# Kernel tuning notes

Hardware: AMD Instinct MI355X
Metric: run time of the kernel (lower is better)

Reference implementation:

```python
import jax, jax.numpy as jnp
import numpy as np

D = 128      # embedding_dim
H = 8        # n_heads
L = 2        # n_encode_layers
FF = 512     # feed-forward hidden (4*D, AM default)
CLIP = 10.0  # tanh_clipping
EPS = 1e-5


def setup_inputs() -> dict:
    key = jax.random.key(0)
    ks = jax.random.split(key, 24)
    B, N = 32, 1000
    Nt = N + 2  # 2 depots + customers

    def w(k, shape, fan_in):
        return (jax.random.normal(k, shape, jnp.float32) / np.float32(np.sqrt(fan_in)))

    inp = {}
    inp["depot"] = jax.random.uniform(ks[0], (B, 2, 2), jnp.float32)
    inp["loc"] = jax.random.uniform(ks[1], (B, N, 2), jnp.float32)
    inp["demand"] = jax.random.uniform(ks[2], (B, N), jnp.float32)
    inp["mask"] = jax.random.randint(ks[3], (B, Nt), 0, 2) == 1
    # init embeddings
    inp["W_init_node"] = w(ks[4], (3, D), 3)
    inp["b_init_node"] = jnp.zeros((D,), jnp.float32)
    inp["W_init_depot"] = w(ks[5], (2, D), 2)
    inp["b_init_depot"] = jnp.zeros((D,), jnp.float32)
    # encoder layers (stacked over L)
    inp["enc_Wqkv"] = w(ks[6], (L, D, 3 * D), D)
    inp["enc_Wo"] = w(ks[7], (L, D, D), D)
    inp["enc_W1"] = w(ks[8], (L, D, FF), D)
    inp["enc_b1"] = jnp.zeros((L, FF), jnp.float32)
    inp["enc_W2"] = w(ks[9], (L, FF, D), FF)
    inp["enc_b2"] = jnp.zeros((L, D), jnp.float32)
    inp["bn1_s"] = jnp.ones((L, D), jnp.float32)
    inp["bn1_b"] = jnp.zeros((L, D), jnp.float32)
    inp["bn2_s"] = jnp.ones((L, D), jnp.float32)
    inp["bn2_b"] = jnp.zeros((L, D), jnp.float32)
    # decoder precompute / pointer attention
    inp["W_proj_node"] = w(ks[10], (D, 3 * D), D)   # project_node_embeddings_p2v
    inp["W_fixed_ctx"] = w(ks[11], (D, D), D)       # project_node_query_context
    inp["W_step_ctx"] = w(ks[12], (D, D), D)        # project_step_context_p2v
    inp["W_out"] = w(ks[13], (D, D), D)             # project_out_p2v
    return inp


def _bn(x, s, b):
    # BatchNorm1d over flattened (batch*nodes), training-mode stats, affine
    m = x.mean((0, 1))
    v = x.var((0, 1))
    return s * (x - m) * jax.lax.rsqrt(v + EPS) + b


def _mha(x, Wqkv, Wo):
    B, N, _ = x.shape
    dk = D // H
    q, k, v = jnp.split(x @ Wqkv, 3, axis=-1)

    def heads(t):
        return t.reshape(B, N, H, dk).transpose(0, 2, 1, 3)  # [B,H,N,dk]

    q, k, v = heads(q), heads(k), heads(v)
    attn = jax.nn.softmax(jnp.einsum('bhqd,bhkd->bhqk', q, k) / np.float32(np.sqrt(dk)), axis=-1)
    o = jnp.einsum('bhqk,bhkd->bhqd', attn, v).transpose(0, 2, 1, 3).reshape(B, N, D)
    return o @ Wo


def reference(depot, loc, demand, mask,
              W_init_node, b_init_node, W_init_depot, b_init_depot,
              enc_Wqkv, enc_Wo, enc_W1, enc_b1, enc_W2, enc_b2,
              bn1_s, bn1_b, bn2_s, bn2_b,
              W_proj_node, W_fixed_ctx, W_step_ctx, W_out):
    B = loc.shape[0]
    NEG = jnp.float32(-1e9)
    # --- init embeddings: depots via Linear(2,D), nodes via Linear(3,D) on (x,y,demand)
    depot_emb = depot @ W_init_depot + b_init_depot                      # [B,2,D]
    node_feat = jnp.concatenate([loc, demand[..., None]], -1)            # [B,N,3]
    node_emb = node_feat @ W_init_node + b_init_node                     # [B,N,D]
    h = jnp.concatenate([depot_emb, node_emb], 1)                        # [B,Nt,D]
    # --- graph encoder: L x (MHA + BN skip, FF + BN skip)
    for l in range(L):
        h = _bn(h + _mha(h, enc_Wqkv[l], enc_Wo[l]), bn1_s[l], bn1_b[l])
        ff = jax.nn.relu(h @ enc_W1[l] + enc_b1[l]) @ enc_W2[l] + enc_b2[l]
        h = _bn(h + ff, bn2_s[l], bn2_b[l])
    # --- fixed precompute (AttentionModelFixed)
    graph_embed = h.mean(1)                                              # [B,D]
    fixed_ctx = graph_embed @ W_fixed_ctx                                # [B,D]
    K_g, V_g, K_logit = jnp.split(h @ W_proj_node, 3, axis=-1)           # each [B,Nt,D]
    dk = D // H
    Kh = K_g.reshape(B, -1, H, dk).transpose(0, 2, 1, 3)                 # [B,H,Nt,dk]
    Vh = V_g.reshape(B, -1, H, dk).transpose(0, 2, 1, 3)
    # --- one glimpse+pointer step: context = fixed + projected first-depot step context
    query = fixed_ctx + h[:, 0, :] @ W_step_ctx                          # [B,D]
    qh = query.reshape(B, H, dk)                                         # [B,H,dk]
    compat = jnp.einsum('bhd,bhnd->bhn', qh, Kh) / np.float32(np.sqrt(dk))
    compat = jnp.where(mask[:, None, :], NEG, compat)                    # mask_inner
    attn = jax.nn.softmax(compat, axis=-1)
    glimpse = jnp.einsum('bhn,bhnd->bhd', attn, Vh).reshape(B, D) @ W_out
    logits = jnp.einsum('bd,bnd->bn', glimpse, K_logit) / np.float32(np.sqrt(D))
    logits = CLIP * jnp.tanh(logits)                                     # tanh clipping
    logits = jnp.where(mask, NEG, logits)                                # mask_logits
    log_p = jax.nn.log_softmax(logits, axis=-1)                          # [B,Nt]
    return log_p
```

## Files before the change

kernel.cpp:

```cpp
#include <hip/hip_runtime.h>

#define B_   32
#define NT_  1002
#define D_   128
#define H_   8
#define FF_  512
#define ROWS (B_ * NT_)
#define NEGV (-1e9f)
#define NTP  1024

typedef __bf16 bf16;
typedef __bf16 bf16x8 __attribute__((ext_vector_type(8)));
typedef __bf16 bf16x4 __attribute__((ext_vector_type(4)));
typedef float  f32x4  __attribute__((ext_vector_type(4)));
typedef float  f32x16 __attribute__((ext_vector_type(16)));

#if __has_builtin(__builtin_amdgcn_exp2f)
#define EXP2(x) __builtin_amdgcn_exp2f(x)
#else
#define EXP2(x) exp2f(x)
#endif

#define MFMA16(a, b, c) __builtin_amdgcn_mfma_f32_16x16x32_bf16(a, b, c, 0, 0, 0)
#define MFMA32(a, b, c) __builtin_amdgcn_mfma_f32_32x32x16_bf16(a, b, c, 0, 0, 0)

__device__ __forceinline__ int UNIT(int row, int seg) {
  return (row >> 4) * 64 + seg * 16 + (row & 15);
}
__device__ __forceinline__ int UNIT128(int row, int seg) {
  return (row >> 4) * 256 + seg * 16 + (row & 15);
}

#define SZ_QKV (2*384*128)
#define SZ_WO  (2*128*128)
#define SZ_W1  (2*512*128)
#define SZ_W2  (2*128*512)
#define SZ_PROJ (384*128)

__global__ __launch_bounds__(256) void prep_w(
    const float* __restrict__ qkv, const float* __restrict__ wo, const float* __restrict__ w1,
    const float* __restrict__ w2, const float* __restrict__ proj, bf16* __restrict__ out) {
  int i = blockIdx.x * 256 + threadIdx.x;
  int j = i;
  float v;
  if (j < SZ_QKV) {
    int l = j / 49152, r = j % 49152; int n = r >> 7, k = r & 127;
    v = qkv[((size_t)l * 128 + k) * 384 + n];
  } else {
    j -= SZ_QKV;
    if (j < SZ_WO) {
      int l = j >> 14, r = j & 16383; int n = r >> 7, k = r & 127;
      v = wo[((size_t)l * 128 + k) * 128 + n];
    } else {
      j -= SZ_WO;
      if (j < SZ_W1) {
        int l = j >> 16, r = j & 65535; int n = r >> 7, k = r & 127;
        v = w1[((size_t)l * 128 + k) * 512 + n];
      } else {
        j -= SZ_W1;
        if (j < SZ_W2) {
          int l = j >> 16, r = j & 65535; int n = r >> 9, k = r & 511;
          v = w2[((size_t)l * 512 + k) * 128 + n];
        } else {
          j -= SZ_W2;
          int n = j >> 7, k = j & 127;
          v = proj[(size_t)k * 384 + n];
        }
      }
    }
  }
  out[i] = (bf16)v;
}

__global__ __launch_bounds__(256) void init_kernel(
    const float* __restrict__ depot, const float* __restrict__ loc, const float* __restrict__ demand,
    const float* __restrict__ Wn, const float* __restrict__ bn_, const float* __restrict__ Wd,
    const float* __restrict__ bd, bf16* __restrict__ hb) {
  int idx = blockIdx.x * 256 + threadIdx.x;
  if (idx >= ROWS * D_) return;
  int c = idx & 127;
  int row = idx >> 7;
  int b = row / NT_;
  int n = row - b * NT_;
  float v;
  if (n < 2) {
    const float* dp = depot + (b * 2 + n) * 2;
    v = dp[0] * Wd[c] + dp[1] * Wd[D_ + c] + bd[c];
  } else {
    int i = n - 2;
    const float* lp = loc + ((size_t)b * 1000 + i) * 2;
    v = lp[0] * Wn[c] + lp[1] * Wn[D_ + c] + demand[b * 1000 + i] * Wn[2 * D_ + c] + bn_[c];
  }
  hb[idx] = (bf16)v;
}

template<int N_, int K_, bool BIAS, bool RELU, bool RES, bool STATS, bool BNA, bool BNR>
__global__ __launch_bounds__(256) void mgemm(
    const bf16* __restrict__ A, const bf16* __restrict__ Wt,
    const float* __restrict__ bias, const bf16* __restrict__ R, bf16* __restrict__ Cout,
    float* __restrict__ ps, float* __restrict__ pq,
    const float* __restrict__ miA, const float* __restrict__ miR) {
  __shared__ bf16 AsF[2048];
  __shared__ bf16 BsF[4096];
  __shared__ float sredS[4][64];
  __shared__ float sredQ[4][64];
  int tid = threadIdx.x;
  int w = tid >> 6, l = tid & 63;
  int bm = blockIdx.y * 64, bn = blockIdx.x * 128;
  int wr = (w >> 1) * 32, wc = (w & 1) * 64;
  f32x4 acc[2][4] = {};
  int srow = tid >> 2, sseg = tid & 3;
  int uA = UNIT(srow, sseg) * 8;
  int uB0 = UNIT(srow, sseg) * 8, uB1 = UNIT(srow + 64, sseg) * 8;
  for (int k0 = 0; k0 < K_; k0 += 32) {
    __syncthreads();
    {
      bf16x8 x = *(const bf16x8*)&A[(size_t)(bm + srow) * K_ + k0 + sseg * 8];
      if (BNA) {
        int kc = k0 + sseg * 8;
        f32x4 s0 = *(const f32x4*)&miA[kc],       s1 = *(const f32x4*)&miA[kc + 4];
        f32x4 c0 = *(const f32x4*)&miA[128 + kc], c1 = *(const f32x4*)&miA[128 + kc + 4];
        bf16x8 y;
#pragma unroll
        for (int i = 0; i < 4; ++i) y[i] = (bf16)__builtin_fmaf((float)x[i], s0[i], c0[i]);
#pragma unroll
        for (int i = 0; i < 4; ++i) y[4 + i] = (bf16)__builtin_fmaf((float)x[4 + i], s1[i], c1[i]);
        *(bf16x8*)&AsF[uA] = y;
      } else {
        *(bf16x8*)&AsF[uA] = x;
      }
    }
    *(bf16x8*)&BsF[uB0] = *(const bf16x8*)&Wt[(size_t)(bn + srow) * K_ + k0 + sseg * 8];
    *(bf16x8*)&BsF[uB1] = *(const bf16x8*)&Wt[(size_t)(bn + srow + 64) * K_ + k0 + sseg * 8];
    __syncthreads();
    bf16x8 af[2], bfr[4];
#pragma unroll
    for (int mi = 0; mi < 2; ++mi)
      af[mi] = *(const bf16x8*)&AsF[(((wr >> 4) + mi) * 64 + (l >> 4) * 16 + (l & 15)) * 8];
#pragma unroll
    for (int ni = 0; ni < 4; ++ni)
      bfr[ni] = *(const bf16x8*)&BsF[(((wc >> 4) + ni) * 64 + (l >> 4) * 16 + (l & 15)) * 8];
#pragma unroll
    for (int mi = 0; mi < 2; ++mi)
#pragma unroll
      for (int ni = 0; ni < 4; ++ni)
        acc[mi][ni] = MFMA16(af[mi], bfr[ni], acc[mi][ni]);
  }
  float scol[4] = {}, qcol[4] = {};
#pragma unroll
  for (int mi = 0; mi < 2; ++mi)
#pragma unroll
    for (int ni = 0; ni < 4; ++ni) {
      int col = bn + wc + ni * 16 + (l & 15);
      float rs = 1.f, rb = 0.f;
      if (RES && BNR) { rs = miR[col]; rb = miR[128 + col]; }
#pragma unroll
      for (int r = 0; r < 4; ++r) {
        int row = bm + wr + mi * 16 + (l >> 4) * 4 + r;
        float v = acc[mi][ni][r];
        if (BIAS) v += bias[col];
        if (RELU) v = fmaxf(v, 0.f);
        if (RES) {
          float x = (float)R[(size_t)row * N_ + col];
          v += BNR ? __builtin_fmaf(x, rs, rb) : x;
        }
        if (STATS) { scol[ni] += v; qcol[ni] += v * v; }
        Cout[(size_t)row * N_ + col] = (bf16)v;
      }
    }
  if (STATS) {
#pragma unroll
    for (int ni = 0; ni < 4; ++ni) {
      scol[ni] += __shfl_xor(scol[ni], 16); scol[ni] += __shfl_xor(scol[ni], 32);
      qcol[ni] += __shfl_xor(qcol[ni], 16); qcol[ni] += __shfl_xor(qcol[ni], 32);
    }
    __syncthreads();
    if (l < 16) {
#pragma unroll
      for (int ni = 0; ni < 4; ++ni) {
        sredS[w][ni * 16 + l] = scol[ni];
        sredQ[w][ni * 16 + l] = qcol[ni];
      }
    }
    __syncthreads();
    if (tid < 128) {
      int c = tid, cw = c >> 6, cc = c & 63;
      ps[(size_t)(bn + c) * 512 + blockIdx.y] = sredS[cw][cc] + sredS[cw + 2][cc];
      pq[(size_t)(bn + c) * 512 + blockIdx.y] = sredQ[cw][cc] + sredQ[cw + 2][cc];
    }
  }
}

template<bool BNA>
__global__ __launch_bounds__(256) void mgemm_qkv(
    const bf16* __restrict__ A, const bf16* __restrict__ Wt, const float* __restrict__ miA,
    bf16* __restrict__ Qh, bf16* __restrict__ Kh, bf16* __restrict__ Vh) {
  __shared__ bf16 smem[128 * 68];
  bf16* AsF = smem;
  bf16* BsF = smem + 2048;
  bf16* Vt2 = smem;
  int tid = threadIdx.x;
  int w = tid >> 6, l = tid & 63;
  int bm = blockIdx.y * 64, bn = blockIdx.x * 128;
  int wr = (w >> 1) * 32, wc = (w & 1) * 64;
  f32x4 acc[2][4] = {};
  int srow = tid >> 2, sseg = tid & 3;
  int uA = UNIT(srow, sseg) * 8;
  int uB0 = UNIT(srow, sseg) * 8, uB1 = UNIT(srow + 64, sseg) * 8;
  for (int k0 = 0; k0 < 128; k0 += 32) {
    __syncthreads();
    {
      bf16x8 x = *(const bf16x8*)&A[(size_t)(bm + srow) * 128 + k0 + sseg * 8];
      if (BNA) {
        int kc = k0 + sseg * 8;
        f32x4 s0 = *(const f32x4*)&miA[kc],       s1 = *(const f32x4*)&miA[kc + 4];
        f32x4 c0 = *(const f32x4*)&miA[128 + kc], c1 = *(const f32x4*)&miA[128 + kc + 4];
        bf16x8 y;
#pragma unroll
        for (int i = 0; i < 4; ++i) y[i] = (bf16)__builtin_fmaf((float)x[i], s0[i], c0[i]);
#pragma unroll
        for (int i = 0; i < 4; ++i) y[4 + i] = (bf16)__builtin_fmaf((float)x[4 + i], s1[i], c1[i]);
        *(bf16x8*)&AsF[uA] = y;
      } else {
        *(bf16x8*)&AsF[uA] = x;
      }
    }
    *(bf16x8*)&BsF[uB0] = *(const bf16x8*)&Wt[(size_t)(bn + srow) * 128 + k0 + sseg * 8];
    *(bf16x8*)&BsF[uB1] = *(const bf16x8*)&Wt[(size_t)(bn + srow + 64) * 128 + k0 + sseg * 8];
    __syncthreads();
    bf16x8 af[2], bfr[4];
#pragma unroll
    for (int mi = 0; mi < 2; ++mi)
      af[mi] = *(const bf16x8*)&AsF[(((wr >> 4) + mi) * 64 + (l >> 4) * 16 + (l & 15)) * 8];
#pragma unroll
    for (int ni = 0; ni < 4; ++ni)
      bfr[ni] = *(const bf16x8*)&BsF[(((wc >> 4) + ni) * 64 + (l >> 4) * 16 + (l & 15)) * 8];
#pragma unroll
    for (int mi = 0; mi < 2; ++mi)
#pragma unroll
      for (int ni = 0; ni < 4; ++ni)
        acc[mi][ni] = MFMA16(af[mi], bfr[ni], acc[mi][ni]);
  }
  if (blockIdx.x < 2) {
    bf16* dst = (blockIdx.x == 0) ? Qh : Kh;
    float qs = (blockIdx.x == 0) ? 0.36067376022224085f : 1.0f;
#pragma unroll
    for (int ni = 0; ni < 4; ++ni) {
      int cl = wc + ni * 16 + (l & 15);
      int hd = cl >> 4, c16 = cl & 15;
#pragma unroll
      for (int mi = 0; mi < 2; ++mi)
#pragma unroll
        for (int r = 0; r < 4; ++r) {
          int row = bm + wr + mi * 16 + (l >> 4) * 4 + r;
          int b = row / NT_;
          int n = row - b * NT_;
          dst[(((size_t)b * 8 + hd) * NTP + n) * 16 + c16] = (bf16)(acc[mi][ni][r] * qs);
        }
    }
  } else {
    __syncthreads();
#pragma unroll
    for (int mi = 0; mi < 2; ++mi)
#pragma unroll
      for (int ni = 0; ni < 4; ++ni) {
        int cl = wc + ni * 16 + (l & 15);
        int r0 = wr + mi * 16 + (l >> 4) * 4;
        bf16x4 pk;
#pragma unroll
        for (int r = 0; r < 4; ++r) pk[r] = (bf16)acc[mi][ni][r];
        *(bf16x4*)&Vt2[cl * 68 + r0] = pk;
      }
    __syncthreads();
    int colg = tid >> 4, nl = tid & 15;
#pragma unroll
    for (int ci = 0; ci < 8; ++ci) {
      int lc = colg + ci * 16;
      int hd = lc >> 4, c16 = lc & 15;
#pragma unroll
      for (int ri = 0; ri < 4; ++ri) {
        int lrow = nl + ri * 16;
        int row = bm + lrow;
        int b = row / NT_;
        int n = row - b * NT_;
        Vh[(((size_t)b * 8 + hd) * 16 + c16) * NTP + n] = Vt2[lc * 68 + lrow];
      }
    }
  }
}

__global__ __launch_bounds__(256) void fffused(
    const bf16* __restrict__ X, const float* __restrict__ mi,
    const bf16* __restrict__ W1t, const float* __restrict__ bias1,
    const bf16* __restrict__ W2t, const float* __restrict__ bias2,
    bf16* __restrict__ Y, float* __restrict__ ps, float* __restrict__ pq) {
  __shared__ bf16 A1[8192];
  __shared__ bf16 A2[8192];
  __shared__ bf16 BF[4096];
  __shared__ float sredS[4][64];
  __shared__ float sredQ[4][64];
  int tid = threadIdx.x;
  int w = tid >> 6, l = tid & 63;
  int bm = blockIdx.x * 64;
#pragma unroll
  for (int it = 0; it < 4; ++it) {
    int idx = it * 256 + tid;
    int row = idx >> 4, seg = idx & 15;
    bf16x8 x = *(const bf16x8*)&X[(size_t)(bm + row) * 128 + seg * 8];
    f32x4 s0 = *(const f32x4*)&mi[seg * 8],       s1 = *(const f32x4*)&mi[seg * 8 + 4];
    f32x4 c0 = *(const f32x4*)&mi[128 + seg * 8], c1 = *(const f32x4*)&mi[128 + seg * 8 + 4];
    bf16x8 y;
#pragma unroll
    for (int i = 0; i < 4; ++i) y[i] = (bf16)__builtin_fmaf((float)x[i], s0[i], c0[i]);
#pragma unroll
    for (int i = 0; i < 4; ++i) y[4 + i] = (bf16)__builtin_fmaf((float)x[4 + i], s1[i], c1[i]);
    *(bf16x8*)&A1[UNIT128(row, seg) * 8] = y;
  }
  int srow = tid >> 2, sseg = tid & 3;
  int uB0 = UNIT(srow, sseg) * 8, uB1 = UNIT(srow + 64, sseg) * 8;
  int wr = (w >> 1) * 32, wc = (w & 1) * 64;
  f32x4 acc2[2][4] = {};

  for (int nc = 0; nc < 4; ++nc) {
    f32x4 acc1[2][4] = {};
    for (int k0 = 0; k0 < 128; k0 += 32) {
      __syncthreads();
      *(bf16x8*)&BF[uB0] = *(const bf16x8*)&W1t[(size_t)(nc * 128 + srow) * 128 + k0 + sseg * 8];
      *(bf16x8*)&BF[uB1] = *(const bf16x8*)&W1t[(size_t)(nc * 128 + srow + 64) * 128 + k0 + sseg * 8];
      __syncthreads();
      bf16x8 af[2], hf[4];
#pragma unroll
      for (int m2 = 0; m2 < 2; ++m2)
        af[m2] = *(const bf16x8*)&BF[((w * 2 + m2) * 64 + (l >> 4) * 16 + (l & 15)) * 8];
#pragma unroll
      for (int ni = 0; ni < 4; ++ni)
        hf[ni] = *(const bf16x8*)&A1[(ni * 256 + ((k0 >> 3) + (l >> 4)) * 16 + (l & 15)) * 8];
#pragma unroll
      for (int m2 = 0; m2 < 2; ++m2)
#pragma unroll
        for (int ni = 0; ni < 4; ++ni)
          acc1[m2][ni] = MFMA16(af[m2], hf[ni], acc1[m2][ni]);
    }
#pragma unroll
    for (int m2 = 0; m2 < 2; ++m2) {
      int ffk0 = w * 32 + m2 * 16 + (l >> 4) * 4;
      int seg = ffk0 >> 3, half = ffk0 & 7;
#pragma unroll
      for (int ni = 0; ni < 4; ++ni) {
        bf16x4 pk;
#pragma unroll
        for (int r = 0; r < 4; ++r) {
          float v = acc1[m2][ni][r] + bias1[nc * 128 + ffk0 + r];
          pk[r] = (bf16)fmaxf(v, 0.f);
        }
        *(bf16x4*)&A2[(ni * 256 + seg * 16 + (l & 15)) * 8 + half] = pk;
      }
    }
    __syncthreads();
    for (int k0 = 0; k0 < 128; k0 += 32) {
      if (k0) __syncthreads();
      *(bf16x8*)&BF[uB0] = *(const bf16x8*)&W2t[(size_t)srow * 512 + nc * 128 + k0 + sseg * 8];
      *(bf16x8*)&BF[uB1] = *(const bf16x8*)&W2t[(size_t)(srow + 64) * 512 + nc * 128 + k0 + sseg * 8];
      __syncthreads();
      bf16x8 a2f[2], b2f[4];
#pragma unroll
      for (int m2 = 0; m2 < 2; ++m2)
        a2f[m2] = *(const bf16x8*)&A2[(((wr >> 4) + m2) * 256 + ((k0 >> 3) + (l >> 4)) * 16 + (l & 15)) * 8];
#pragma unroll
      for (int ni = 0; ni < 4; ++ni)
        b2f[ni] = *(const bf16x8*)&BF[(((wc >> 4) + ni) * 64 + (l >> 4) * 16 + (l & 15)) * 8];
#pragma unroll
      for (int m2 = 0; m2 < 2; ++m2)
#pragma unroll
        for (int ni = 0; ni < 4; ++ni)
          acc2[m2][ni] = MFMA16(a2f[m2], b2f[ni], acc2[m2][ni]);
    }
  }
  float scol[4] = {}, qcol[4] = {};
#pragma unroll
  for (int m2 = 0; m2 < 2; ++m2)
#pragma unroll
    for (int ni = 0; ni < 4; ++ni) {
      int col = wc + ni * 16 + (l & 15);
      float bb = bias2[col];
#pragma unroll
      for (int r = 0; r < 4; ++r) {
        int row = wr + m2 * 16 + (l >> 4) * 4 + r;
        float res = (float)A1[UNIT128(row, col >> 3) * 8 + (col & 7)];
        float v = acc2[m2][ni][r] + bb + res;
        scol[ni] += v; qcol[ni] += v * v;
        Y[(size_t)(bm + row) * 128 + col] = (bf16)v;
      }
    }
#pragma unroll
  for (int ni = 0; ni < 4; ++ni) {
    scol[ni] += __shfl_xor(scol[ni], 16); scol[ni] += __shfl_xor(scol[ni], 32);
    qcol[ni] += __shfl_xor(qcol[ni], 16); qcol[ni] += __shfl_xor(qcol[ni], 32);
  }
  __syncthreads();
  if (l < 16) {
#pragma unroll
    for (int ni = 0; ni < 4; ++ni) {
      sredS[w][ni * 16 + l] = scol[ni];
      sredQ[w][ni * 16 + l] = qcol[ni];
    }
  }
  __syncthreads();
  if (tid < 128) {
    int c = tid, cw = c >> 6, cc = c & 63;
    ps[(size_t)c * 512 + blockIdx.x] = sredS[cw][cc] + sredS[cw + 2][cc];
    pq[(size_t)c * 512 + blockIdx.x] = sredQ[cw][cc] + sredQ[cw + 2][cc];
  }
}

__global__ __launch_bounds__(256) void mattn(
    const bf16* __restrict__ Qh, const bf16* __restrict__ Kh,
    const bf16* __restrict__ Vh, bf16* __restrict__ ab) {
  __shared__ bf16 KsF[1024];
  __shared__ bf16 VtF[1024];
  __shared__ bf16 PsF[4][2048];
  int tid = threadIdx.x;
  int w = tid >> 6, l = tid & 63;
  int bh = blockIdx.x;
  int b = bh >> 3, hd = bh & 7;
  const bf16* Qp = Qh + (size_t)bh * NTP * 16;
  const bf16* Kp = Kh + (size_t)bh * NTP * 16;
  const bf16* Vp = Vh + (size_t)bh * 16 * NTP;
  int qbase = blockIdx.y * 128 + w * 32;
  int qrow = qbase + (l & 31); if (qrow >= NT_) qrow = NT_ - 1;
  bf16x8 qf = *(const bf16x8*)&Qp[qrow * 16 + (l >> 5) * 8];

  f32x4 oacc[2] = {};
  f32x4 lacc[2] = {};
  bf16x8 ones;
#pragma unroll
  for (int i = 0; i < 8; ++i) ones[i] = (bf16)1.0f;
  const f32x16 zz = {0,0,0,0,0,0,0,0,0,0,0,0,0,0,0,0};

  for (int t = 0; t < 16; ++t) {
    int kb = t * 64;
    __syncthreads();
    if (tid < 128) {
      int key = (tid >> 6) * 32 + (tid & 31);
      int h2 = (tid >> 5) & 1;
      int krow = kb + key; if (krow >= NT_) krow = NT_ - 1;
      *(bf16x8*)&KsF[tid * 8] = *(const bf16x8*)&Kp[krow * 16 + h2 * 8];
    } else {
      int u = tid - 128;
      int seg = u >> 4, dim = u & 15;
      *(bf16x8*)&VtF[u * 8] = *(const bf16x8*)&Vp[dim * NTP + kb + seg * 8];
    }
    __syncthreads();

    f32x16 sv[2];
    __builtin_amdgcn_s_setprio(1);
#pragma unroll
    for (int c = 0; c < 2; ++c) {
      bf16x8 kf = *(const bf16x8*)&KsF[(c * 64 + l) * 8];
      sv[c] = MFMA32(kf, qf, zz);
    }
    __builtin_amdgcn_s_setprio(0);
    if (kb + 64 > NT_) {
#pragma unroll
      for (int c = 0; c < 2; ++c)
#pragma unroll
        for (int r = 0; r < 16; ++r) {
          int key = kb + c * 32 + (r & 3) + 8 * (r >> 2) + 4 * (l >> 5);
          if (key >= NT_) sv[c][r] = -1e30f;
        }
    }
#pragma unroll
    for (int c = 0; c < 2; ++c)
#pragma unroll
      for (int r = 0; r < 16; ++r)
        sv[c][r] = EXP2(sv[c][r]);
    {
      int q = l & 31;
      int qh4 = q >> 4, ql = q & 15, half = (l >> 5) * 4;
#pragma unroll
      for (int c = 0; c < 2; ++c)
#pragma unroll
        for (int g2 = 0; g2 < 4; ++g2) {
          bf16x4 pk;
#pragma unroll
          for (int i = 0; i < 4; ++i) pk[i] = (bf16)sv[c][g2 * 4 + i];
          int unit = (c * 2 + qh4) * 64 + g2 * 16 + ql;
          *(bf16x4*)&PsF[w][unit * 8 + half] = pk;
        }
    }
    __builtin_amdgcn_s_setprio(1);
#pragma unroll
    for (int kh = 0; kh < 2; ++kh) {
      bf16x8 vf = *(const bf16x8*)&VtF[(kh * 64 + l) * 8];
#pragma unroll
      for (int g = 0; g < 2; ++g) {
        bf16x8 pf = *(const bf16x8*)&PsF[w][((kh * 2 + g) * 64 + l) * 8];
        oacc[g] = MFMA16(pf, vf, oacc[g]);
        lacc[g] = MFMA16(pf, ones, lacc[g]);
      }
    }
    __builtin_amdgcn_s_setprio(0);
  }
#pragma unroll
  for (int g = 0; g < 2; ++g)
#pragma unroll
    for (int r = 0; r < 4; ++r) {
      int qq = qbase + g * 16 + (l >> 4) * 4 + r;
      if (qq < NT_)
        ab[((size_t)b * NT_ + qq) * 128 + hd * 16 + (l & 15)] = (bf16)(oacc[g][r] / lacc[g][r]);
    }
}

__global__ __launch_bounds__(512) void stats_final(
    const float* __restrict__ ps, const float* __restrict__ pq,
    const float* __restrict__ sc, const float* __restrict__ bi, float* __restrict__ mi) {
  int tid = threadIdx.x;
  int c = tid >> 2, q4 = tid & 3;
  float s = 0.f, q = 0.f;
  for (int p = q4; p < 501; p += 4) { s += ps[c * 512 + p]; q += pq[c * 512 + p]; }
  s += __shfl_xor(s, 1); s += __shfl_xor(s, 2);
  q += __shfl_xor(q, 1); q += __shfl_xor(q, 2);
  if (q4 == 0) {
    float mean = s * (1.f / (float)ROWS);
    float var = q * (1.f / (float)ROWS) - mean * mean;
    float s2 = sc[c] * rsqrtf(var + 1e-5f);
    mi[c] = s2;
    mi[128 + c] = bi[c] - mean * s2;
  }
}

__global__ void ge_partial(const bf16* __restrict__ X, const float* __restrict__ mi,
                           float* __restrict__ part) {
  int b = blockIdx.x, ch = blockIdx.y, d = threadIdx.x;
  int n0 = ch * 126, n1 = n0 + 126; if (n1 > NT_) n1 = NT_;
  float sS = mi[d], sB = mi[128 + d];
  float s = 0.f;
  for (int n = n0; n < n1; ++n)
    s += __builtin_fmaf((float)X[((size_t)b * NT_ + n) * D_ + d], sS, sB);
  part[(b * 8 + ch) * D_ + d] = s;
}

__global__ void query_kernel(const float* __restrict__ part, const bf16* __restrict__ X,
                             const float* __restrict__ mi,
                             const float* __restrict__ Wf, const float* __restrict__ Ws,
                             float* __restrict__ qry) {
  __shared__ float sge[128], sh0[128];
  int b = blockIdx.x, d = threadIdx.x;
  float s = 0.f;
#pragma unroll
  for (int ch = 0; ch < 8; ++ch) s += part[(b * 8 + ch) * D_ + d];
  sge[d] = s * (1.f / (float)NT_);
  sh0[d] = __builtin_fmaf((float)X[(size_t)b * NT_ * D_ + d], mi[d], mi[128 + d]);
  __syncthreads();
  float q = 0.f;
  for (int k = 0; k < 128; ++k) q += sge[k] * Wf[k * D_ + d] + sh0[k] * Ws[k * D_ + d];
  qry[b * D_ + d] = q;
}

__global__ __launch_bounds__(256) void glimpse_kernel(
    const bf16* __restrict__ proj, const float* __restrict__ qry,
    const int* __restrict__ mask, float* __restrict__ glimpse) {
  int bid = blockIdx.x; int b = bid >> 3, hd = bid & 7;
  int tid = threadIdx.x;
  __shared__ float sq[16];
  __shared__ float sex[NT_];
  __shared__ float rmax[4];
  __shared__ float wacc[4][17];
  if (tid < 16) sq[tid] = qry[b * 128 + hd * 16 + tid];
  __syncthreads();
  const bf16* P = proj + (size_t)b * NT_ * 384;
  const int* Mk = mask + b * NT_;
  float lmax = -1e30f;
#pragma unroll
  for (int it = 0; it < 4; ++it) {
    int n = tid + it * 256;
    if (n < NT_) {
      float c = NEGV;
      if (!Mk[n]) {
        const bf16* kp = &P[(size_t)n * 384 + hd * 16];
        bf16x8 k0 = *(const bf16x8*)kp, k1 = *(const bf16x8*)(kp + 8);
        float d = 0.f;
#pragma unroll
        for (int i = 0; i < 8; ++i) d += sq[i] * (float)k0[i] + sq[8 + i] * (float)k1[i];
        c = d * 0.25f;
      }
      sex[n] = c;
      lmax = fmaxf(lmax, c);
    }
  }
#pragma unroll
  for (int o = 32; o > 0; o >>= 1) lmax = fmaxf(lmax, __shfl_xor(lmax, o));
  if ((tid & 63) == 0) rmax[tid >> 6] = lmax;
  __syncthreads();
  float mx = fmaxf(fmaxf(rmax[0], rmax[1]), fmaxf(rmax[2], rmax[3]));
  float acc[16];
#pragma unroll
  for (int i = 0; i < 16; ++i) acc[i] = 0.f;
  float lsum = 0.f;
#pragma unroll
  for (int it = 0; it < 4; ++it) {
    int n = tid + it * 256;
    if (n < NT_) {
      float e = __expf(sex[n] - mx);
      lsum += e;
      const bf16* vp = &P[(size_t)n * 384 + 128 + hd * 16];
      bf16x8 v0 = *(const bf16x8*)vp, v1 = *(const bf16x8*)(vp + 8);
#pragma unroll
      for (int i = 0; i < 8; ++i) { acc[i] += e * (float)v0[i]; acc[8 + i] += e * (float)v1[i]; }
    }
  }
#pragma unroll
  for (int o = 32; o > 0; o >>= 1) {
    lsum += __shfl_xor(lsum, o);
#pragma unroll
    for (int i = 0; i < 16; ++i) acc[i] += __shfl_xor(acc[i], o);
  }
  if ((tid & 63) == 0) {
    wacc[tid >> 6][16] = lsum;
#pragma unroll
    for (int i = 0; i < 16; ++i) wacc[tid >> 6][i] = acc[i];
  }
  __syncthreads();
  if (tid < 16) {
    float a = wacc[0][tid] + wacc[1][tid] + wacc[2][tid] + wacc[3][tid];
    float L = wacc[0][16] + wacc[1][16] + wacc[2][16] + wacc[3][16];
    glimpse[b * 128 + hd * 16 + tid] = a / L;
  }
}

__global__ void g2_kernel(const float* __restrict__ glimpse, const float* __restrict__ Wout,
                          float* __restrict__ g2) {
  __shared__ float sg[128];
  int b = blockIdx.x, d = threadIdx.x;
  sg[d] = glimpse[b * 128 + d];
  __syncthreads();
  float s = 0.f;
  for (int k = 0; k < 128; ++k) s += sg[k] * Wout[k * 128 + d];
  g2[b * 128 + d] = s;
}

__global__ __launch_bounds__(256) void logits_kernel(
    const bf16* __restrict__ proj, const float* __restrict__ g2,
    const int* __restrict__ mask, float* __restrict__ logits) {
  int b = blockIdx.y;
  int n = blockIdx.x * 256 + threadIdx.x;
  __shared__ float sg[128];
  if (threadIdx.x < 128) sg[threadIdx.x] = g2[b * 128 + threadIdx.x];
  __syncthreads();
  if (n >= NT_) return;
  const bf16* kp = &proj[((size_t)b * NT_ + n) * 384 + 256];
  float d = 0.f;
#pragma unroll
  for (int j = 0; j < 16; ++j) {
    bf16x8 v = *(const bf16x8*)&kp[j * 8];
#pragma unroll
    for (int i = 0; i < 8; ++i) d += sg[j * 8 + i] * (float)v[i];
  }
  d = 10.f * tanhf(d * 0.088388347648318447f);
  logits[b * NT_ + n] = mask[b * NT_ + n] ? NEGV : d;
}

__global__ __launch_bounds__(256) void lsm_kernel(const float* __restrict__ logits, float* __restrict__ out) {
  int b = blockIdx.x, tid = threadIdx.x;
  __shared__ float red[256];
  float mx = -1e30f;
  for (int n = tid; n < NT_; n += 256) mx = fmaxf(mx, logits[b * NT_ + n]);
  red[tid] = mx; __syncthreads();
  for (int s = 128; s > 0; s >>= 1) { if (tid < s) red[tid] = fmaxf(red[tid], red[tid + s]); __syncthreads(); }
  mx = red[0]; __syncthreads();
  float sm = 0.f;
  for (int n = tid; n < NT_; n += 256) sm += __expf(logits[b * NT_ + n] - mx);
  red[tid] = sm; __syncthreads();
  for (int s = 128; s > 0; s >>= 1) { if (tid < s) red[tid] += red[tid + s]; __syncthreads(); }
  float lse = mx + logf(red[0]);
  for (int n = tid; n < NT_; n += 256) out[(size_t)b * NT_ + n] = logits[b * NT_ + n] - lse;
}

extern "C" void kernel_launch(void* const* d_in, const int* in_sizes, int n_in,
                              void* d_out, int out_size, void* d_ws, size_t ws_size,
                              hipStream_t stream) {
  const float* depot        = (const float*)d_in[0];
  const float* loc          = (const float*)d_in[1];
  const float* demand       = (const float*)d_in[2];
  const int*   mask         = (const int*)d_in[3];
  const float* W_init_node  = (const float*)d_in[4];
  const float* b_init_node  = (const float*)d_in[5];
  const float* W_init_depot = (const float*)d_in[6];
  const float* b_init_depot = (const float*)d_in[7];
  const float* enc_Wqkv     = (const float*)d_in[8];
  const float* enc_Wo       = (const float*)d_in[9];
  const float* enc_W1       = (const float*)d_in[10];
  const float* enc_b1       = (const float*)d_in[11];
  const float* enc_W2       = (const float*)d_in[12];
  const float* enc_b2       = (const float*)d_in[13];
  const float* bn1_s        = (const float*)d_in[14];
  const float* bn1_b        = (const float*)d_in[15];
  const float* bn2_s        = (const float*)d_in[16];
  const float* bn2_b        = (const float*)d_in[17];
  const float* W_proj       = (const float*)d_in[18];
  const float* W_fixed      = (const float*)d_in[19];
  const float* W_step       = (const float*)d_in[20];
  const float* W_out        = (const float*)d_in[21];
  float* out = (float*)d_out;

  char* base = (char*)d_ws;
  bf16*  hb0   = (bf16*)(base);
  bf16*  ab    = (bf16*)(base + 8208384);
  bf16*  Qh    = (bf16*)(base + 16416768);
  bf16*  Kh    = (bf16*)(base + 24805376);
  bf16*  Vh    = (bf16*)(base + 33193984);
  bf16*  xb1   = Qh;
  bf16*  xb2   = (bf16*)(base + 41582592);
  bf16*  projb = (bf16*)(base + 49790976);
  bf16*  wb    = (bf16*)(base + 74416128);
  float* ps    = (float*)(base + 75300864);
  float* pq    = (float*)(base + 75563008);
  float* mi1   = (float*)(base + 75825152);
  float* mi2   = (float*)(base + 75826176);
  float* qry   = (float*)(base + 75827200);
  float* glim  = (float*)(base + 75843584);
  float* g2    = (float*)(base + 75859968);
  float* gep   = ps;
  float* logit = pq;

  bf16* wt_qkv  = wb;
  bf16* wt_wo   = wb + SZ_QKV;
  bf16* wt_w1   = wb + SZ_QKV + SZ_WO;
  bf16* wt_w2   = wb + SZ_QKV + SZ_WO + SZ_W1;
  bf16* wt_proj = wb + SZ_QKV + SZ_WO + SZ_W1 + SZ_W2;

  prep_w<<<1728, 256, 0, stream>>>(enc_Wqkv, enc_Wo, enc_W1, enc_W2, W_proj, wb);
  init_kernel<<<(ROWS * D_ + 255) / 256, 256, 0, stream>>>(
      depot, loc, demand, W_init_node, b_init_node, W_init_depot, b_init_depot, hb0);

  for (int l = 0; l < 2; ++l) {
    const bf16* hin = (l == 0) ? hb0 : xb2;
    if (l == 0)
      mgemm_qkv<false><<<dim3(3, 501), 256, 0, stream>>>(hin, wt_qkv, nullptr, Qh, Kh, Vh);
    else
      mgemm_qkv<true><<<dim3(3, 501), 256, 0, stream>>>(hin, wt_qkv + (size_t)384 * 128, mi2, Qh, Kh, Vh);
    mattn<<<dim3(256, 8), 256, 0, stream>>>(Qh, Kh, Vh, ab);
    if (l == 0)
      mgemm<128, 128, false, false, true, true, false, false><<<dim3(1, 501), 256, 0, stream>>>(
          ab, wt_wo, nullptr, hin, xb1, ps, pq, nullptr, nullptr);
    else
      mgemm<128, 128, false, false, true, true, false, true><<<dim3(1, 501), 256, 0, stream>>>(
          ab, wt_wo + (size_t)128 * 128, nullptr, hin, xb1, ps, pq, nullptr, mi2);
    stats_final<<<1, 512, 0, stream>>>(ps, pq, bn1_s + l * D_, bn1_b + l * D_, mi1);
    fffused<<<501, 256, 0, stream>>>(
        xb1, mi1, wt_w1 + (size_t)l * 512 * 128, enc_b1 + (size_t)l * FF_,
        wt_w2 + (size_t)l * 128 * 512, enc_b2 + (size_t)l * D_, xb2, ps, pq);
    stats_final<<<1, 512, 0, stream>>>(ps, pq, bn2_s + l * D_, bn2_b + l * D_, mi2);
  }

  mgemm<384, 128, false, false, false, false, true, false><<<dim3(3, 501), 256, 0, stream>>>(
      xb2, wt_proj, nullptr, nullptr, projb, nullptr, nullptr, mi2, nullptr);
  ge_partial<<<dim3(32, 8), 128, 0, stream>>>(xb2, mi2, gep);
  query_kernel<<<32, 128, 0, stream>>>(gep, xb2, mi2, W_fixed, W_step, qry);
  glimpse_kernel<<<256, 256, 0, stream>>>(projb, qry, mask, glim);
  g2_kernel<<<32, 128, 0, stream>>>(glim, W_out, g2);
  logits_kernel<<<dim3(4, 32), 256, 0, stream>>>(projb, g2, mask, logit);
  lsm_kernel<<<32, 256, 0, stream>>>(logit, out);
}
```

Baseline: 359.8 us.

## Tile weight transpose, prefetch attention K/V tiles, fuse pointer tail kernels

Weight preparation now transposes through a shared-memory 64x64 tile, so both the fp32 reads and the bf16 writes are coalesced, replacing the strided per-element gather. The attention kernel keeps the next K/V tile in registers while the current tile is being computed, so the global-load latency overlaps with the MFMA work. The g2 projection, logits and log-softmax kernels are merged into one per-batch kernel that keeps the logits in shared memory, which removes two launches and a global round trip. In exchange, the fused tail runs on only 32 blocks, so the logits computation has less parallelism than before.

```diff
diff --git a/kernel.cpp b/kernel.cpp
--- a/kernel.cpp
+++ b/kernel.cpp
@@ -40,36 +40,38 @@
 __global__ __launch_bounds__(256) void prep_w(
     const float* __restrict__ qkv, const float* __restrict__ wo, const float* __restrict__ w1,
     const float* __restrict__ w2, const float* __restrict__ proj, bf16* __restrict__ out) {
-  int i = blockIdx.x * 256 + threadIdx.x;
-  int j = i;
-  float v;
-  if (j < SZ_QKV) {
-    int l = j / 49152, r = j % 49152; int n = r >> 7, k = r & 127;
-    v = qkv[((size_t)l * 128 + k) * 384 + n];
+  __shared__ float tile[64][65];
+  int bid = blockIdx.x;
+  const float* src; bf16* dst; int K, N, kt, nt;
+  if (bid < 24) {
+    int l = bid / 12, r = bid % 12; kt = r / 6; nt = r % 6; K = 128; N = 384;
+    src = qkv + (size_t)l * 128 * 384; dst = out + (size_t)l * 49152;
+  } else if (bid < 32) {
+    int q = bid - 24; int l = q / 4, r = q % 4; kt = r / 2; nt = r % 2; K = 128; N = 128;
+    src = wo + (size_t)l * 16384; dst = out + SZ_QKV + (size_t)l * 16384;
+  } else if (bid < 64) {
+    int q = bid - 32; int l = q / 16, r = q % 16; kt = r / 8; nt = r % 8; K = 128; N = 512;
+    src = w1 + (size_t)l * 65536; dst = out + SZ_QKV + SZ_WO + (size_t)l * 65536;
+  } else if (bid < 96) {
+    int q = bid - 64; int l = q / 16, r = q % 16; kt = r / 2; nt = r % 2; K = 512; N = 128;
+    src = w2 + (size_t)l * 65536; dst = out + SZ_QKV + SZ_WO + SZ_W1 + (size_t)l * 65536;
   } else {
-    j -= SZ_QKV;
-    if (j < SZ_WO) {
-      int l = j >> 14, r = j & 16383; int n = r >> 7, k = r & 127;
-      v = wo[((size_t)l * 128 + k) * 128 + n];
-    } else {
-      j -= SZ_WO;
-      if (j < SZ_W1) {
-        int l = j >> 16, r = j & 65535; int n = r >> 7, k = r & 127;
-        v = w1[((size_t)l * 128 + k) * 512 + n];
-      } else {
-        j -= SZ_W1;
-        if (j < SZ_W2) {
-          int l = j >> 16, r = j & 65535; int n = r >> 9, k = r & 511;
-          v = w2[((size_t)l * 512 + k) * 128 + n];
-        } else {
-          j -= SZ_W2;
-          int n = j >> 7, k = j & 127;
-          v = proj[(size_t)k * 384 + n];
-        }
-      }
-    }
-  }
-  out[i] = (bf16)v;
+    int r = bid - 96; kt = r / 6; nt = r % 6; K = 128; N = 384;
+    src = proj; dst = out + SZ_QKV + SZ_WO + SZ_W1 + SZ_W2;
+  }
+  int k0 = kt * 64, n0 = nt * 64;
+  int tx = threadIdx.x & 63, ty = threadIdx.x >> 6;
+#pragma unroll
+  for (int it = 0; it < 16; ++it) {
+    int row = it * 4 + ty;
+    tile[row][tx] = src[(size_t)(k0 + row) * N + n0 + tx];
+  }
+  __syncthreads();
+#pragma unroll
+  for (int it = 0; it < 16; ++it) {
+    int row = it * 4 + ty;
+    dst[(size_t)(n0 + row) * K + k0 + tx] = (bf16)tile[tx][row];
+  }
 }
 
 __global__ __launch_bounds__(256) void init_kernel(
@@ -437,20 +439,34 @@
   for (int i = 0; i < 8; ++i) ones[i] = (bf16)1.0f;
   const f32x16 zz = {0,0,0,0,0,0,0,0,0,0,0,0,0,0,0,0};
 
+  int skey = 0, sh2 = 0, svseg = 0, svdim = 0;
+  bf16x8 stg;
+  if (tid < 128) {
+    skey = (tid >> 6) * 32 + (tid & 31);
+    sh2 = (tid >> 5) & 1;
+    int krow = skey; if (krow >= NT_) krow = NT_ - 1;
+    stg = *(const bf16x8*)&Kp[krow * 16 + sh2 * 8];
+  } else {
+    int u = tid - 128;
+    svseg = u >> 4; svdim = u & 15;
+    stg = *(const bf16x8*)&Vp[svdim * NTP + svseg * 8];
+  }
+
   for (int t = 0; t < 16; ++t) {
     int kb = t * 64;
     __syncthreads();
-    if (tid < 128) {
-      int key = (tid >> 6) * 32 + (tid & 31);
-      int h2 = (tid >> 5) & 1;
-      int krow = kb + key; if (krow >= NT_) krow = NT_ - 1;
-      *(bf16x8*)&KsF[tid * 8] = *(const bf16x8*)&Kp[krow * 16 + h2 * 8];
-    } else {
-      int u = tid - 128;
-      int seg = u >> 4, dim = u & 15;
-      *(bf16x8*)&VtF[u * 8] = *(const bf16x8*)&Vp[dim * NTP + kb + seg * 8];
-    }
-    __syncthreads();
+    if (tid < 128) *(bf16x8*)&KsF[tid * 8] = stg;
+    else           *(bf16x8*)&VtF[(tid - 128) * 8] = stg;
+    __syncthreads();
+    if (t < 15) {
+      int kb2 = kb + 64;
+      if (tid < 128) {
+        int krow = kb2 + skey; if (krow >= NT_) krow = NT_ - 1;
+        stg = *(const bf16x8*)&Kp[krow * 16 + sh2 * 8];
+      } else {
+        stg = *(const bf16x8*)&Vp[svdim * NTP + kb2 + svseg * 8];
+      }
+    }
 
     f32x16 sv[2];
     __builtin_amdgcn_s_setprio(1);
@@ -628,52 +644,46 @@
   }
 }
 
-__global__ void g2_kernel(const float* __restrict__ glimpse, const float* __restrict__ Wout,
-                          float* __restrict__ g2) {
+__global__ __launch_bounds__(256) void ptr_tail(
+    const float* __restrict__ glim, const float* __restrict__ Wout,
+    const bf16* __restrict__ proj, const int* __restrict__ mask, float* __restrict__ out) {
   __shared__ float sg[128];
-  int b = blockIdx.x, d = threadIdx.x;
-  sg[d] = glimpse[b * 128 + d];
-  __syncthreads();
-  float s = 0.f;
-  for (int k = 0; k < 128; ++k) s += sg[k] * Wout[k * 128 + d];
-  g2[b * 128 + d] = s;
-}
-
-__global__ __launch_bounds__(256) void logits_kernel(
-    const bf16* __restrict__ proj, const float* __restrict__ g2,
-    const int* __restrict__ mask, float* __restrict__ logits) {
-  int b = blockIdx.y;
-  int n = blockIdx.x * 256 + threadIdx.x;
-  __shared__ float sg[128];
-  if (threadIdx.x < 128) sg[threadIdx.x] = g2[b * 128 + threadIdx.x];
-  __syncthreads();
-  if (n >= NT_) return;
-  const bf16* kp = &proj[((size_t)b * NT_ + n) * 384 + 256];
-  float d = 0.f;
-#pragma unroll
-  for (int j = 0; j < 16; ++j) {
-    bf16x8 v = *(const bf16x8*)&kp[j * 8];
-#pragma unroll
-    for (int i = 0; i < 8; ++i) d += sg[j * 8 + i] * (float)v[i];
-  }
-  d = 10.f * tanhf(d * 0.088388347648318447f);
-  logits[b * NT_ + n] = mask[b * NT_ + n] ? NEGV : d;
-}
-
-__global__ __launch_bounds__(256) void lsm_kernel(const float* __restrict__ logits, float* __restrict__ out) {
+  __shared__ float sg2[128];
+  __shared__ float slog[NT_];
+  __shared__ float red[256];
   int b = blockIdx.x, tid = threadIdx.x;
-  __shared__ float red[256];
+  if (tid < 128) sg[tid] = glim[b * 128 + tid];
+  __syncthreads();
+  if (tid < 128) {
+    float s = 0.f;
+    for (int k = 0; k < 128; ++k) s += sg[k] * Wout[k * 128 + tid];
+    sg2[tid] = s;
+  }
+  __syncthreads();
+  for (int n = tid; n < NT_; n += 256) {
+    const bf16* kp = &proj[((size_t)b * NT_ + n) * 384 + 256];
+    float d = 0.f;
+#pragma unroll
+    for (int j = 0; j < 16; ++j) {
+      bf16x8 v = *(const bf16x8*)&kp[j * 8];
+#pragma unroll
+      for (int i = 0; i < 8; ++i) d += sg2[j * 8 + i] * (float)v[i];
+    }
+    d = 10.f * tanhf(d * 0.088388347648318447f);
+    slog[n] = mask[b * NT_ + n] ? NEGV : d;
+  }
+  __syncthreads();
   float mx = -1e30f;
-  for (int n = tid; n < NT_; n += 256) mx = fmaxf(mx, logits[b * NT_ + n]);
+  for (int n = tid; n < NT_; n += 256) mx = fmaxf(mx, slog[n]);
   red[tid] = mx; __syncthreads();
   for (int s = 128; s > 0; s >>= 1) { if (tid < s) red[tid] = fmaxf(red[tid], red[tid + s]); __syncthreads(); }
   mx = red[0]; __syncthreads();
   float sm = 0.f;
-  for (int n = tid; n < NT_; n += 256) sm += __expf(logits[b * NT_ + n] - mx);
+  for (int n = tid; n < NT_; n += 256) sm += __expf(slog[n] - mx);
   red[tid] = sm; __syncthreads();
   for (int s = 128; s > 0; s >>= 1) { if (tid < s) red[tid] += red[tid + s]; __syncthreads(); }
   float lse = mx + logf(red[0]);
-  for (int n = tid; n < NT_; n += 256) out[(size_t)b * NT_ + n] = logits[b * NT_ + n] - lse;
+  for (int n = tid; n < NT_; n += 256) out[(size_t)b * NT_ + n] = slog[n] - lse;
 }
 
 extern "C" void kernel_launch(void* const* d_in, const int* in_sizes, int n_in,
@@ -719,9 +729,7 @@
   float* mi2   = (float*)(base + 75826176);
   float* qry   = (float*)(base + 75827200);
   float* glim  = (float*)(base + 75843584);
-  float* g2    = (float*)(base + 75859968);
   float* gep   = ps;
-  float* logit = pq;
 
   bf16* wt_qkv  = wb;
   bf16* wt_wo   = wb + SZ_QKV;
@@ -729,7 +737,7 @@
   bf16* wt_w2   = wb + SZ_QKV + SZ_WO + SZ_W1;
   bf16* wt_proj = wb + SZ_QKV + SZ_WO + SZ_W1 + SZ_W2;
 
-  prep_w<<<1728, 256, 0, stream>>>(enc_Wqkv, enc_Wo, enc_W1, enc_W2, W_proj, wb);
+  prep_w<<<108, 256, 0, stream>>>(enc_Wqkv, enc_Wo, enc_W1, enc_W2, W_proj, wb);
   init_kernel<<<(ROWS * D_ + 255) / 256, 256, 0, stream>>>(
       depot, loc, demand, W_init_node, b_init_node, W_init_depot, b_init_depot, hb0);
 
@@ -758,7 +766,5 @@
   ge_partial<<<dim3(32, 8), 128, 0, stream>>>(xb2, mi2, gep);
   query_kernel<<<32, 128, 0, stream>>>(gep, xb2, mi2, W_fixed, W_step, qry);
   glimpse_kernel<<<256, 256, 0, stream>>>(projb, qry, mask, glim);
-  g2_kernel<<<32, 128, 0, stream>>>(glim, W_out, g2);
-  logits_kernel<<<dim3(4, 32), 256, 0, stream>>>(projb, g2, mask, logit);
-  lsm_kernel<<<32, 256, 0, stream>>>(logit, out);
-}
+  ptr_tail<<<32, 256, 0, stream>>>(glim, W_out, projb, mask, out);
+}
```

Measured after the change: 366.1 us. No clear change (+1.7%).
